# Kernel optimization log

Measured on AMD Instinct MI355X. Metric: run time of the kernel, lower is better.

The kernel has to match this reference:

```python
import math
import jax
import jax.numpy as jnp
import numpy as np

IMAGE_SIZE = 256
FOV_DEG = 60.0
NEAR, FAR = 0.01, 10.0
CHUNK = 128          # faces processed per scan step (bounds peak memory)
BIG_Z = 1e10         # 'infinite' depth for empty pixels


def _projection_matrix():
    f = 1.0 / math.tan(math.radians(FOV_DEG) / 2)
    return jnp.array([
        [f, 0.0, 0.0, 0.0],
        [0.0, f, 0.0, 0.0],
        [0.0, 0.0, (FAR + NEAR) / (NEAR - FAR), 2.0 * FAR * NEAR / (NEAR - FAR)],
        [0.0, 0.0, -1.0, 0.0],
    ], dtype=jnp.float32)


def _rasterize_mask(v_ndc, faces):
    """Coverage mask via edge-function triangle rasterization with a z-buffer.
    v_ndc: [V,3] ndc coords, faces: [F,3] int. Returns float [H,W] mask."""
    H = W = IMAGE_SIZE
    dt = v_ndc.dtype
    px = ((jnp.arange(W, dtype=dt) + 0.5) / W * 2.0 - 1.0)[None, None, :]  # [1,1,W]
    py = ((jnp.arange(H, dtype=dt) + 0.5) / H * 2.0 - 1.0)[None, :, None]  # [1,H,1]
    fchunks = faces.reshape(-1, CHUNK, 3)

    def body(carry, fc):
        zbuf, mask = carry
        tri = v_ndc[fc]  # [C,3,3]
        x0 = tri[:, 0, 0][:, None, None]; y0 = tri[:, 0, 1][:, None, None]; z0 = tri[:, 0, 2][:, None, None]
        x1 = tri[:, 1, 0][:, None, None]; y1 = tri[:, 1, 1][:, None, None]; z1 = tri[:, 1, 2][:, None, None]
        x2 = tri[:, 2, 0][:, None, None]; y2 = tri[:, 2, 1][:, None, None]; z2 = tri[:, 2, 2][:, None, None]
        # edge functions, [C,H,W]
        e0 = (x1 - x0) * (py - y0) - (y1 - y0) * (px - x0)
        e1 = (x2 - x1) * (py - y1) - (y2 - y1) * (px - x1)
        e2 = (x0 - x2) * (py - y2) - (y0 - y2) * (px - x2)
        inside = ((e0 >= 0) & (e1 >= 0) & (e2 >= 0)) | ((e0 <= 0) & (e1 <= 0) & (e2 <= 0))
        area = e0 + e1 + e2
        denom = jnp.where(jnp.abs(area) > 1e-12, area, 1.0)
        # barycentric-interpolated depth
        z = (e1 * z0 + e2 * z1 + e0 * z2) / denom
        zc = jnp.where(inside, z, BIG_Z)
        zbuf = jnp.minimum(zbuf, jnp.min(zc, axis=0))
        mask = jnp.maximum(mask, jnp.max(inside.astype(dt), axis=0))
        return (zbuf, mask), None

    zbuf0 = jnp.full((H, W), BIG_Z, dtype=dt)
    mask0 = jnp.zeros((H, W), dtype=dt)
    (_, mask), _ = jax.lax.scan(body, (zbuf0, mask0), fchunks)
    return mask


def setup_inputs() -> dict:
    key = jax.random.key(0)
    k1, k2, k3, k4 = jax.random.split(key, 4)
    B, V, F = 2, 4096, 4096
    verts = jax.random.normal(k1, (B, V, 3), dtype=jnp.float32)
    faces = jax.random.randint(k2, (B, F, 3), 0, V, dtype=jnp.int64 if jax.config.jax_enable_x64 else jnp.int32)
    R = jax.random.normal(k3, (B, 3, 3), dtype=jnp.float32)
    T = jax.random.normal(k4, (B, 3), dtype=jnp.float32)
    return {"verts": verts, "faces": faces, "R": R, "T": T}


def reference(verts, faces, R, T):
    proj = _projection_matrix()
    # world2cam: [R^T | -R^T t] with homogeneous bottom row, built batched
    Rt = jnp.swapaxes(R, -1, -2)                       # [B,3,3]
    t = -jnp.einsum('bij,bj->bi', Rt, T)               # [B,3]
    top = jnp.concatenate([Rt, t[..., None]], axis=-1)  # [B,3,4]
    bottom = jnp.broadcast_to(jnp.array([[0.0, 0.0, 0.0, 1.0]], dtype=verts.dtype), (R.shape[0], 1, 4))
    w2c = jnp.concatenate([top, bottom], axis=1)       # [B,4,4]
    VP = jnp.einsum('ij,bjk->bik', proj, w2c)          # [B,4,4]
    homo = jnp.concatenate([verts, jnp.ones_like(verts[..., :1])], axis=-1)  # [B,V,4]
    cam = jnp.einsum('bvk,bjk->bvj', homo, VP)         # verts_homo @ VP.T
    ndc = cam[..., :3] / jnp.maximum(cam[..., 3:], 1e-8)  # clamp(min=1e-8)
    mask = jax.vmap(_rasterize_mask)(ndc, faces)       # [B,H,W]
    return jnp.repeat(mask[..., None], 3, axis=-1)     # [B,H,W,3]
```

## Files before the change

### kernel.cpp

```cpp
#include <hip/hip_runtime.h>


#pragma clang fp contract(off)

#define HW      256
#define BATCH   2
#define VCOUNT  4096
#define FCOUNT  4096
#define CHUNK_F 512

__global__ __launch_bounds__(256)
void vert_kernel(const float* __restrict__ verts,
                 const float* __restrict__ R,
                 const float* __restrict__ T,
                 float2* __restrict__ ndc)
{
#pragma clang fp contract(off)
    int gid = blockIdx.x * blockDim.x + threadIdx.x;
    if (gid >= BATCH * VCOUNT) return;
    int b = gid / VCOUNT;

    const float fproj = 1.7320508075688772f;

    const float* Rb = R + b * 9;
    const float* Tb = T + b * 3;

    float t0 = -((Rb[0*3+0]*Tb[0] + Rb[1*3+0]*Tb[1]) + Rb[2*3+0]*Tb[2]);
    float t1 = -((Rb[0*3+1]*Tb[0] + Rb[1*3+1]*Tb[1]) + Rb[2*3+1]*Tb[2]);
    float t2 = -((Rb[0*3+2]*Tb[0] + Rb[1*3+2]*Tb[1]) + Rb[2*3+2]*Tb[2]);

    float VP00 = fproj * Rb[0*3+0], VP01 = fproj * Rb[1*3+0],
          VP02 = fproj * Rb[2*3+0], VP03 = fproj * t0;
    float VP10 = fproj * Rb[0*3+1], VP11 = fproj * Rb[1*3+1],
          VP12 = fproj * Rb[2*3+1], VP13 = fproj * t1;
    float VP30 = -Rb[0*3+2], VP31 = -Rb[1*3+2],
          VP32 = -Rb[2*3+2], VP33 = -t2;

    const float* vv = verts + (size_t)gid * 3;
    float vx = vv[0], vy = vv[1], vz = vv[2];

    float cx = ((vx*VP00 + vy*VP01) + vz*VP02) + VP03;
    float cy = ((vx*VP10 + vy*VP11) + vz*VP12) + VP13;
    float cw = ((vx*VP30 + vy*VP31) + vz*VP32) + VP33;

    float w = fmaxf(cw, 1e-8f);
    ndc[gid] = make_float2(cx / w, cy / w);
}

__global__ __launch_bounds__(256)
void raster_kernel(const float2* __restrict__ ndc,
                   const int* __restrict__ faces,
                   float* __restrict__ out)
{
#pragma clang fp contract(off)
    __shared__ float4 sf[CHUNK_F * 3];

    int b    = blockIdx.y;
    int tile = blockIdx.x;
    int px_i = ((tile & 15) << 4) + (threadIdx.x & 15);
    int py_i = ((tile >> 4) << 4) + (threadIdx.x >> 4);

    float px = (((float)px_i + 0.5f) / 256.0f) * 2.0f - 1.0f;
    float py = (((float)py_i + 0.5f) / 256.0f) * 2.0f - 1.0f;

    const float2* nb = ndc + b * VCOUNT;
    const int*    fb = faces + b * FCOUNT * 3;

    bool covered = false;

    for (int c0 = 0; c0 < FCOUNT; c0 += CHUNK_F) {
        for (int t = threadIdx.x; t < CHUNK_F; t += 256) {
            const int* fp = fb + (size_t)(c0 + t) * 3;
            int i0 = fp[0], i1 = fp[1], i2 = fp[2];
            float2 p0 = nb[i0], p1 = nb[i1], p2 = nb[i2];
            sf[t*3 + 0] = make_float4(p0.x, p0.y, p1.x, p1.y);
            sf[t*3 + 1] = make_float4(p2.x, p2.y, p1.x - p0.x, p1.y - p0.y);
            sf[t*3 + 2] = make_float4(p2.x - p1.x, p2.y - p1.y,
                                      p0.x - p2.x, p0.y - p2.y);
        }
        __syncthreads();

        for (int f8 = 0; f8 < CHUNK_F; f8 += 8) {
            if (__all((int)covered)) break;
#pragma unroll
            for (int k = 0; k < 8; ++k) {
                int f = f8 + k;
                float4 a = sf[f*3 + 0];
                float4 c = sf[f*3 + 1];
                float4 d = sf[f*3 + 2];
                float e0 = c.z * (py - a.y) - c.w * (px - a.x);
                float e1 = d.x * (py - a.w) - d.y * (px - a.z);
                float e2 = d.z * (py - c.y) - d.w * (px - c.x);
                float mn = fminf(fminf(e0, e1), e2);
                float mx = fmaxf(fmaxf(e0, e1), e2);
                covered = covered || (mn >= 0.0f) || (mx <= 0.0f);
            }
        }

        if (__syncthreads_and((int)covered)) break;
    }

    float val = covered ? 1.0f : 0.0f;
    size_t o = ((size_t)(b * HW + py_i) * HW + px_i) * 3;
    out[o + 0] = val;
    out[o + 1] = val;
    out[o + 2] = val;
}

extern "C" void kernel_launch(void* const* d_in, const int* in_sizes, int n_in,
                              void* d_out, int out_size, void* d_ws, size_t ws_size,
                              hipStream_t stream) {
    const float* verts = (const float*)d_in[0];
    const int*   faces = (const int*)d_in[1];
    const float* R     = (const float*)d_in[2];
    const float* T     = (const float*)d_in[3];
    float*       out   = (float*)d_out;

    float2* ndc = (float2*)d_ws;

    int nv = BATCH * VCOUNT;
    vert_kernel<<<(nv + 255) / 256, 256, 0, stream>>>(verts, R, T, ndc);

    dim3 grid(256, BATCH);
    raster_kernel<<<grid, 256, 0, stream>>>(ndc, faces, out);
}
```

Measured before the change: 65.78 us.

## Precompute packed face edge data in first kernel, read directly in raster

The vertex kernel becomes a per-face kernel that gathers the three vertices, projects them, and writes the packed edge coefficients to global memory. The raster kernel drops its shared-memory staging and block barriers and reads the packed faces straight from global memory, relying on cache broadcast since every lane reads the same address. This removes the per-block gather and sync cost, and each wave can now stop on its own once covered instead of waiting for a block-wide check. In exchange, vertex projection is repeated per face (roughly three times the work), and the inner loop uses global or scalar loads in place of LDS reads.

```diff
diff --git a/kernel.cpp b/kernel.cpp
--- a/kernel.cpp
+++ b/kernel.cpp
@@ -7,18 +7,19 @@
 #define BATCH   2
 #define VCOUNT  4096
 #define FCOUNT  4096
-#define CHUNK_F 512
+
 
 __global__ __launch_bounds__(256)
-void vert_kernel(const float* __restrict__ verts,
-                 const float* __restrict__ R,
-                 const float* __restrict__ T,
-                 float2* __restrict__ ndc)
+void face_pack_kernel(const float* __restrict__ verts,
+                      const int* __restrict__ faces,
+                      const float* __restrict__ R,
+                      const float* __restrict__ T,
+                      float4* __restrict__ fpack)
 {
 #pragma clang fp contract(off)
     int gid = blockIdx.x * blockDim.x + threadIdx.x;
-    if (gid >= BATCH * VCOUNT) return;
-    int b = gid / VCOUNT;
+    if (gid >= BATCH * FCOUNT) return;
+    int b = gid / FCOUNT;
 
     const float fproj = 1.7320508075688772f;
 
@@ -36,25 +37,31 @@
     float VP30 = -Rb[0*3+2], VP31 = -Rb[1*3+2],
           VP32 = -Rb[2*3+2], VP33 = -t2;
 
-    const float* vv = verts + (size_t)gid * 3;
-    float vx = vv[0], vy = vv[1], vz = vv[2];
+    const int* fp = faces + (size_t)gid * 3;
+    float xs[3], ys[3];
+#pragma unroll
+    for (int j = 0; j < 3; ++j) {
+        const float* vv = verts + ((size_t)b * VCOUNT + fp[j]) * 3;
+        float vx = vv[0], vy = vv[1], vz = vv[2];
+        float cx = ((vx*VP00 + vy*VP01) + vz*VP02) + VP03;
+        float cy = ((vx*VP10 + vy*VP11) + vz*VP12) + VP13;
+        float cw = ((vx*VP30 + vy*VP31) + vz*VP32) + VP33;
+        float w = fmaxf(cw, 1e-8f);
+        xs[j] = cx / w;
+        ys[j] = cy / w;
+    }
 
-    float cx = ((vx*VP00 + vy*VP01) + vz*VP02) + VP03;
-    float cy = ((vx*VP10 + vy*VP11) + vz*VP12) + VP13;
-    float cw = ((vx*VP30 + vy*VP31) + vz*VP32) + VP33;
-
-    float w = fmaxf(cw, 1e-8f);
-    ndc[gid] = make_float2(cx / w, cy / w);
+    float4* o = fpack + (size_t)gid * 3;
+    o[0] = make_float4(xs[0], ys[0], xs[1], ys[1]);
+    o[1] = make_float4(xs[2], ys[2], xs[1] - xs[0], ys[1] - ys[0]);
+    o[2] = make_float4(xs[2] - xs[1], ys[2] - ys[1], xs[0] - xs[2], ys[0] - ys[2]);
 }
 
 __global__ __launch_bounds__(256)
-void raster_kernel(const float2* __restrict__ ndc,
-                   const int* __restrict__ faces,
+void raster_kernel(const float4* __restrict__ fpack,
                    float* __restrict__ out)
 {
 #pragma clang fp contract(off)
-    __shared__ float4 sf[CHUNK_F * 3];
-
     int b    = blockIdx.y;
     int tile = blockIdx.x;
     int px_i = ((tile & 15) << 4) + (threadIdx.x & 15);
@@ -63,41 +70,25 @@
     float px = (((float)px_i + 0.5f) / 256.0f) * 2.0f - 1.0f;
     float py = (((float)py_i + 0.5f) / 256.0f) * 2.0f - 1.0f;
 
-    const float2* nb = ndc + b * VCOUNT;
-    const int*    fb = faces + b * FCOUNT * 3;
+    const float4* fb = fpack + (size_t)b * FCOUNT * 3;
 
     bool covered = false;
 
-    for (int c0 = 0; c0 < FCOUNT; c0 += CHUNK_F) {
-        for (int t = threadIdx.x; t < CHUNK_F; t += 256) {
-            const int* fp = fb + (size_t)(c0 + t) * 3;
-            int i0 = fp[0], i1 = fp[1], i2 = fp[2];
-            float2 p0 = nb[i0], p1 = nb[i1], p2 = nb[i2];
-            sf[t*3 + 0] = make_float4(p0.x, p0.y, p1.x, p1.y);
-            sf[t*3 + 1] = make_float4(p2.x, p2.y, p1.x - p0.x, p1.y - p0.y);
-            sf[t*3 + 2] = make_float4(p2.x - p1.x, p2.y - p1.y,
-                                      p0.x - p2.x, p0.y - p2.y);
+    for (int f8 = 0; f8 < FCOUNT; f8 += 8) {
+        if (__all((int)covered)) break;
+#pragma unroll
+        for (int k = 0; k < 8; ++k) {
+            const float4* q = fb + (size_t)(f8 + k) * 3;
+            float4 a = q[0];
+            float4 c = q[1];
+            float4 d = q[2];
+            float e0 = c.z * (py - a.y) - c.w * (px - a.x);
+            float e1 = d.x * (py - a.w) - d.y * (px - a.z);
+            float e2 = d.z * (py - c.y) - d.w * (px - c.x);
+            float mn = fminf(fminf(e0, e1), e2);
+            float mx = fmaxf(fmaxf(e0, e1), e2);
+            covered = covered || (mn >= 0.0f) || (mx <= 0.0f);
         }
-        __syncthreads();
-
-        for (int f8 = 0; f8 < CHUNK_F; f8 += 8) {
-            if (__all((int)covered)) break;
-#pragma unroll
-            for (int k = 0; k < 8; ++k) {
-                int f = f8 + k;
-                float4 a = sf[f*3 + 0];
-                float4 c = sf[f*3 + 1];
-                float4 d = sf[f*3 + 2];
-                float e0 = c.z * (py - a.y) - c.w * (px - a.x);
-                float e1 = d.x * (py - a.w) - d.y * (px - a.z);
-                float e2 = d.z * (py - c.y) - d.w * (px - c.x);
-                float mn = fminf(fminf(e0, e1), e2);
-                float mx = fmaxf(fmaxf(e0, e1), e2);
-                covered = covered || (mn >= 0.0f) || (mx <= 0.0f);
-            }
-        }
-
-        if (__syncthreads_and((int)covered)) break;
     }
 
     float val = covered ? 1.0f : 0.0f;
@@ -116,11 +107,11 @@
     const float* T     = (const float*)d_in[3];
     float*       out   = (float*)d_out;
 
-    float2* ndc = (float2*)d_ws;
+    float4* fpack = (float4*)d_ws;
 
-    int nv = BATCH * VCOUNT;
-    vert_kernel<<<(nv + 255) / 256, 256, 0, stream>>>(verts, R, T, ndc);
+    int nf = BATCH * FCOUNT;
+    face_pack_kernel<<<(nf + 255) / 256, 256, 0, stream>>>(verts, faces, R, T, fpack);
 
     dim3 grid(256, BATCH);
-    raster_kernel<<<grid, 256, 0, stream>>>(ndc, faces, out);
+    raster_kernel<<<grid, 256, 0, stream>>>(fpack, out);
 }
```

Measured after the change: 65.67 us. No clear change (-0.2%).
